# Kernel optimization log

Measured on AMD Instinct MI355X. Metric: run time of the kernel, lower is better.

## Reference

```python
import jax, jax.numpy as jnp
import numpy as np

B, T, C = 2, 2048, 1024
H = 16
D = C // H  # 64

def setup_inputs() -> dict:
    key = jax.random.key(0)
    k1, k2, k3 = jax.random.split(key, 3)
    s = 0.02
    return {
        "x": jax.random.normal(k1, (B, T, C), dtype=jnp.float32),
        "Wqkv": jax.random.normal(k2, (C, 3 * C), dtype=jnp.float32) * s,
        "bqkv": jnp.zeros((3 * C,), dtype=jnp.float32),
        "Wproj": jax.random.normal(k3, (C, C), dtype=jnp.float32) * s,
        "bproj": jnp.zeros((C,), dtype=jnp.float32),
    }

def reference(x, Wqkv, bqkv, Wproj, bproj):
    b, t, c = x.shape
    qkv = x @ Wqkv + bqkv                       # [B,T,3C]
    qkv = qkv.reshape(b, t, 3, H, D)
    q = qkv[:, :, 0].transpose(0, 2, 1, 3)      # [B,H,T,D]
    k = qkv[:, :, 1].transpose(0, 2, 1, 3)
    v = qkv[:, :, 2].transpose(0, 2, 1, 3)
    scale = 1.0 / np.sqrt(D).astype(np.float32)
    att = jnp.einsum('bhqd,bhkd->bhqk', q, k) * scale  # [B,H,T,T]
    causal = jnp.tril(jnp.ones((t, t), dtype=bool))
    att = jnp.where(causal[None, None], att, jnp.float32(-jnp.inf))
    att = jax.nn.softmax(att, axis=-1)
    y = jnp.einsum('bhqk,bhkd->bhqd', att, v)   # [B,H,T,D]
    y = y.transpose(0, 2, 1, 3).reshape(b, t, c)
    return y @ Wproj + bproj
```

## Files before the change

### kernel.cpp

```cpp
#include <hip/hip_runtime.h>

typedef __bf16 bf16x8 __attribute__((ext_vector_type(8)));
typedef float  f32x4  __attribute__((ext_vector_type(4)));
typedef float  f32x16 __attribute__((ext_vector_type(16)));
typedef unsigned int uint32x4 __attribute__((ext_vector_type(4)));

__device__ __forceinline__ short f2bf(float f) {
  union { float f; unsigned u; } v; v.f = f;
  unsigned r = v.u + 0x7fffu + ((v.u >> 16) & 1u);
  return (short)(r >> 16);
}

__device__ __forceinline__ void gl_lds16(const short* g, short* l) {
  __builtin_amdgcn_global_load_lds((const __attribute__((address_space(1))) void*)g,
                                   (__attribute__((address_space(3))) void*)l, 16, 0, 0);
}

__global__ __launch_bounds__(256) void cast_x_kernel(const float* __restrict__ in,
                                                     short* __restrict__ out, int n4) {
  int i = blockIdx.x * 256 + threadIdx.x;
  if (i >= n4) return;
  float4 f = reinterpret_cast<const float4*>(in)[i];
  short4 o;
  o.x = f2bf(f.x); o.y = f2bf(f.y); o.z = f2bf(f.z); o.w = f2bf(f.w);
  reinterpret_cast<short4*>(out)[i] = o;
}

__global__ __launch_bounds__(256) void transpose_cast(const float* __restrict__ in,
                                                      short* __restrict__ out, int R, int Cc) {
  __shared__ short tile[64][65];
  int bx = blockIdx.x * 64;
  int by = blockIdx.y * 64;
  int tx = threadIdx.x & 63, ty = threadIdx.x >> 6;
  #pragma unroll
  for (int i = ty; i < 64; i += 4)
    tile[i][tx] = f2bf(in[(size_t)(by + i) * Cc + bx + tx]);
  __syncthreads();
  #pragma unroll
  for (int i = ty; i < 64; i += 4)
    out[(size_t)(bx + i) * R + by + tx] = tile[tx][i];
}


__global__ __launch_bounds__(512, 1) void gemm_qkv(const short* __restrict__ A,
                                                   const short* __restrict__ Bt,
                                                   const float* __restrict__ bias,
                                                   short* __restrict__ qo,
                                                   short* __restrict__ ko,
                                                   short* __restrict__ vt) {
  const int K = 1024;
  __shared__ short smem[65536];
  int tid = threadIdx.x;
  int g = blockIdx.x;
  int mtile = (g & 15) * 256, ntile = (g >> 4) * 256;
  int w = tid >> 6, l = tid & 63;
  int wr = w >> 2, wc = w & 3;
  int lr = l & 15, lg = l >> 4;

  f32x4 zero4 = {0.f, 0.f, 0.f, 0.f};
  f32x4 acc[8][4];
  #pragma unroll
  for (int i = 0; i < 8; ++i)
    #pragma unroll
    for (int j = 0; j < 4; ++j) acc[i][j] = zero4;

#define STAGE_QKV(BUF, K0) do {                                                      \
    short* Ab_ = smem + (BUF) * 32768;                                               \
    short* Bb_ = Ab_ + 16384;                                                        \
    _Pragma("unroll")                                                                \
    for (int c = 0; c < 4; ++c) {                                                    \
      int idx = tid + c * 512;                                                       \
      int row = idx >> 3, kc = (idx & 7) ^ (row & 7);       \
      gl_lds16(&A[(size_t)(mtile + row) * K + (K0) + kc * 8], &Ab_[idx * 8]);        \
      gl_lds16(&Bt[(size_t)(ntile + row) * K + (K0) + kc * 8], &Bb_[idx * 8]);       \
    }                                                                                \
  } while (0)

  STAGE_QKV(0, 0);
  __syncthreads();
  int cur = 0;
  for (int it = 0; it < 16; ++it) {
    if (it < 15) STAGE_QKV(cur ^ 1, (it + 1) * 64);
    const short* Ab = smem + cur * 32768;
    const short* Bb = Ab + 16384;
    __builtin_amdgcn_s_setprio(1);
    #pragma unroll
    for (int kk = 0; kk < 2; ++kk) {
      bf16x8 af[8], bfr[4];
      #pragma unroll
      for (int i = 0; i < 8; ++i) {
        int rA = wr * 128 + i * 16 + lr;
        af[i] = *reinterpret_cast<const bf16x8*>(&Ab[rA * 64 + (((kk * 4 + lg) ^ (rA & 7)) * 8)]);
      }
      #pragma unroll
      for (int j = 0; j < 4; ++j) {
        int rB = wc * 64 + j * 16 + lr;
        bfr[j] = *reinterpret_cast<const bf16x8*>(&Bb[rB * 64 + (((kk * 4 + lg) ^ (rB & 7)) * 8)]);
      }
      #pragma unroll
      for (int i = 0; i < 8; ++i)
        #pragma unroll
        for (int j = 0; j < 4; ++j)
          acc[i][j] = __builtin_amdgcn_mfma_f32_16x16x32_bf16(af[i], bfr[j], acc[i][j], 0, 0, 0);
    }
    __builtin_amdgcn_s_setprio(0);
    __syncthreads();
    cur ^= 1;
  }
#undef STAGE_QKV

  const int sec = ntile >> 10;
  if (sec == 2) {
    #pragma unroll
    for (int j = 0; j < 4; ++j) {
      int nl = wc * 64 + j * 16 + lr;
      int d  = nl & 63;
      float bv = bias[ntile + nl];
      #pragma unroll
      for (int i = 0; i < 8; ++i) {
        int lt0 = wr * 128 + i * 16 + lg * 4;
        int c2 = (nl >> 6) * 8 + (lt0 >> 5);
        int pos = (((lt0 >> 3) & 1) << 10) + (d & 31) * 32 +
                  ((((lt0 >> 4) & 1) + ((d >> 5) << 1)) << 3) + (lt0 & 7);
        short4 pk;
        pk.x = f2bf(acc[i][j][0] + bv);
        pk.y = f2bf(acc[i][j][1] + bv);
        pk.z = f2bf(acc[i][j][2] + bv);
        pk.w = f2bf(acc[i][j][3] + bv);
        *reinterpret_cast<short4*>(&smem[c2 * 2048 + pos]) = pk;
      }
    }
  } else {
    const float sc = (sec == 0) ? 0.18033688f : 1.0f;
    #pragma unroll
    for (int j = 0; j < 4; ++j) {
      int nl = wc * 64 + j * 16 + lr;
      int d  = nl & 63;
      float bv = bias[ntile + nl];
      int dpart = (((d >> 3) & 1) << 10) + ((d >> 4) << 3) + (d & 7);
      #pragma unroll
      for (int i = 0; i < 8; ++i) {
        #pragma unroll
        for (int r2 = 0; r2 < 4; ++r2) {
          int lt = wr * 128 + i * 16 + lg * 4 + r2;
          int c2 = (nl >> 6) * 8 + (lt >> 5);
          smem[c2 * 2048 + (lt & 31) * 32 + dpart] = f2bf((acc[i][j][r2] + bv) * sc);
        }
      }
    }
  }
  __syncthreads();
  short* dst = (sec == 0) ? qo : ((sec == 1) ? ko : vt);
  int bb  = mtile >> 11;
  int h0  = (ntile & 1023) >> 6;
  int gt0 = (mtile & 2047) >> 5;
  #pragma unroll
  for (int c2 = 0; c2 < 32; ++c2) {
    size_t base = (size_t)(bb * 16 + h0 + (c2 >> 3)) * 131072 +
                  (size_t)(gt0 + (c2 & 7)) * 2048;
    *reinterpret_cast<uint2*>(&dst[base + tid * 4]) =
        *reinterpret_cast<const uint2*>(&smem[c2 * 2048 + tid * 4]);
  }
}

template<int DIAG>
__device__ __forceinline__ void attn_step(const short* __restrict__ kp,
                                          const short* __restrict__ vp,
                                          const bf16x8* qf,
                                          f32x16& y0, f32x16& y1,
                                          float& m, float& li,
                                          int lq, int hl) {
  f32x16 s;
  #pragma unroll
  for (int r = 0; r < 16; ++r) s[r] = 0.f;
  __builtin_amdgcn_s_setprio(1);
  #pragma unroll
  for (int ks = 0; ks < 4; ++ks) {
    bf16x8 kf = *reinterpret_cast<const bf16x8*>(kp + ks * 8);
    s = __builtin_amdgcn_mfma_f32_32x32x16_bf16(kf, qf[ks], s, 0, 0, 0);
  }
  __builtin_amdgcn_s_setprio(0);
  if (DIAG) {
    #pragma unroll
    for (int r = 0; r < 16; ++r) {
      int kvl = (r & 3) + 8 * (r >> 2) + 4 * hl;
      if (kvl > lq) s[r] = -1e30f;
    }
  }
  float a0 = fmaxf(fmaxf(s[0], s[1]), fmaxf(s[2], s[3]));
  float a1 = fmaxf(fmaxf(s[4], s[5]), fmaxf(s[6], s[7]));
  float a2 = fmaxf(fmaxf(s[8], s[9]), fmaxf(s[10], s[11]));
  float a3 = fmaxf(fmaxf(s[12], s[13]), fmaxf(s[14], s[15]));
  float pm = fmaxf(fmaxf(a0, a1), fmaxf(a2, a3));
  pm = fmaxf(pm, __shfl_xor(pm, 32));
  if (!__all(pm - m <= 8.0f)) {
    float mn = fmaxf(m, pm);
    float sc = __builtin_amdgcn_exp2f(m - mn);
    m = mn;
    li *= sc;
    #pragma unroll
    for (int r = 0; r < 16; ++r) { y0[r] *= sc; y1[r] *= sc; }
  }
  unsigned u[8];
  float rs = 0.f;
  #pragma unroll
  for (int rq = 0; rq < 4; ++rq) {
    float p0 = __builtin_amdgcn_exp2f(s[4 * rq + 0] - m);
    float p1 = __builtin_amdgcn_exp2f(s[4 * rq + 1] - m);
    float p2 = __builtin_amdgcn_exp2f(s[4 * rq + 2] - m);
    float p3 = __builtin_amdgcn_exp2f(s[4 * rq + 3] - m);
    rs += (p0 + p1) + (p2 + p3);
    asm("v_cvt_pk_bf16_f32 %0, %1, %2" : "=v"(u[rq * 2 + 0]) : "v"(p0), "v"(p1));
    asm("v_cvt_pk_bf16_f32 %0, %1, %2" : "=v"(u[rq * 2 + 1]) : "v"(p2), "v"(p3));
  }
  rs += __shfl_xor(rs, 32);
  li += rs;
  asm volatile("v_permlane32_swap_b32 %0, %1" : "+v"(u[0]), "+v"(u[2]));
  asm volatile("v_permlane32_swap_b32 %0, %1" : "+v"(u[1]), "+v"(u[3]));
  asm volatile("v_permlane32_swap_b32 %0, %1" : "+v"(u[4]), "+v"(u[6]));
  asm volatile("v_permlane32_swap_b32 %0, %1" : "+v"(u[5]), "+v"(u[7]));
  uint32x4 w0 = {u[0], u[1], u[2], u[3]};
  uint32x4 w1 = {u[4], u[5], u[6], u[7]};
  bf16x8 pa0 = __builtin_bit_cast(bf16x8, w0);
  bf16x8 pa1 = __builtin_bit_cast(bf16x8, w1);
  __builtin_amdgcn_s_setprio(1);
  {
    bf16x8 vf00 = *reinterpret_cast<const bf16x8*>(vp);
    bf16x8 vf01 = *reinterpret_cast<const bf16x8*>(vp + 8);
    bf16x8 vf10 = *reinterpret_cast<const bf16x8*>(vp + 16);
    bf16x8 vf11 = *reinterpret_cast<const bf16x8*>(vp + 24);
    y0 = __builtin_amdgcn_mfma_f32_32x32x16_bf16(vf00, pa0, y0, 0, 0, 0);
    y0 = __builtin_amdgcn_mfma_f32_32x32x16_bf16(vf01, pa1, y0, 0, 0, 0);
    y1 = __builtin_amdgcn_mfma_f32_32x32x16_bf16(vf10, pa0, y1, 0, 0, 0);
    y1 = __builtin_amdgcn_mfma_f32_32x32x16_bf16(vf11, pa1, y1, 0, 0, 0);
  }
  __builtin_amdgcn_s_setprio(0);
}

__global__ __launch_bounds__(256, 4) void attn_kernel(const short* __restrict__ q,
                                                      const short* __restrict__ k,
                                                      const short* __restrict__ vt,
                                                      short* __restrict__ y) {
  __shared__ float partL[3][4][64][4];
  __shared__ float stm[4][32], stl[4][32];
  const int bid = blockIdx.x;
  const int t = 63 - (bid >> 5);
  const int b5 = bid & 31;
  const int bh = (b5 & 7) * 4 + (b5 >> 3);
  const int tid = threadIdx.x;
  const int w = tid >> 6;
  const int l = tid & 63;
  const int lq = l & 31, hl = l >> 5;
  const short* qb = q + (size_t)bh * 131072;
  const short* kb = k + (size_t)bh * 131072;
  const short* vb = vt + (size_t)bh * 131072;

  bf16x8 qf[4];
  {
    const short* qp = qb + (size_t)t * 2048 + l * 32;
    #pragma unroll
    for (int ks = 0; ks < 4; ++ks)
      qf[ks] = *reinterpret_cast<const bf16x8*>(qp + ks * 8);
  }

  f32x16 y0, y1;
  #pragma unroll
  for (int r = 0; r < 16; ++r) { y0[r] = 0.f; y1[r] = 0.f; }
  float m = -1e30f, li = 0.f;

  const short* kp = kb + (size_t)w * 2048 + l * 32;
  const short* vp = vb + (size_t)w * 2048 + l * 32;
  for (int it = w; it < t; it += 4) {
    attn_step<0>(kp, vp, qf, y0, y1, m, li, lq, hl);
    kp += 4 * 2048;
    vp += 4 * 2048;
  }
  if ((t & 3) == w) {
    const short* kpd = kb + (size_t)t * 2048 + l * 32;
    const short* vpd = vb + (size_t)t * 2048 + l * 32;
    attn_step<1>(kpd, vpd, qf, y0, y1, m, li, lq, hl);
  }

  if (hl == 0) { stm[w][lq] = m; stl[w][lq] = li; }
  __syncthreads();
  float m0 = stm[0][lq], m1 = stm[1][lq], m2 = stm[2][lq], m3 = stm[3][lq];
  float M = fmaxf(fmaxf(m0, m1), fmaxf(m2, m3));
  float L = stl[0][lq] * __builtin_amdgcn_exp2f(m0 - M) +
            stl[1][lq] * __builtin_amdgcn_exp2f(m1 - M) +
            stl[2][lq] * __builtin_amdgcn_exp2f(m2 - M) +
            stl[3][lq] * __builtin_amdgcn_exp2f(m3 - M);
  float sc = __builtin_amdgcn_exp2f(m - M);
  #pragma unroll
  for (int r = 0; r < 16; ++r) { y0[r] *= sc; y1[r] *= sc; }

  if (w > 0) {
    #pragma unroll
    for (int c = 0; c < 4; ++c) {
      f32x4 v0 = {y0[4 * c + 0], y0[4 * c + 1], y0[4 * c + 2], y0[4 * c + 3]};
      *reinterpret_cast<f32x4*>(&partL[w - 1][c][l][0]) = v0;
    }
  }
  __syncthreads();
  if (w == 0) {
    #pragma unroll
    for (int o = 0; o < 3; ++o)
      #pragma unroll
      for (int c = 0; c < 4; ++c) {
        f32x4 v0 = *reinterpret_cast<const f32x4*>(&partL[o][c][l][0]);
        #pragma unroll
        for (int r = 0; r < 4; ++r) y0[4 * c + r] += v0[r];
      }
  }
  __syncthreads();
  if (w > 0) {
    #pragma unroll
    for (int c = 0; c < 4; ++c) {
      f32x4 v1 = {y1[4 * c + 0], y1[4 * c + 1], y1[4 * c + 2], y1[4 * c + 3]};
      *reinterpret_cast<f32x4*>(&partL[w - 1][c][l][0]) = v1;
    }
  }
  __syncthreads();
  if (w == 0) {
    #pragma unroll
    for (int o = 0; o < 3; ++o)
      #pragma unroll
      for (int c = 0; c < 4; ++c) {
        f32x4 v1 = *reinterpret_cast<const f32x4*>(&partL[o][c][l][0]);
        #pragma unroll
        for (int r = 0; r < 4; ++r) y1[4 * c + r] += v1[r];
      }
    float inv = 1.0f / L;
    int b_ = bh >> 4, h_ = bh & 15;
    short* yrow = &y[(size_t)(b_ * 2048 + 32 * t + lq) * 1024 + h_ * 64];
    #pragma unroll
    for (int dt = 0; dt < 2; ++dt) {
      const f32x16& yy = dt ? y1 : y0;
      #pragma unroll
      for (int rq = 0; rq < 4; ++rq) {
        int d0 = dt * 32 + 8 * rq + 4 * hl;
        uint2 pk;
        pk.x = (unsigned)(unsigned short)f2bf(yy[4 * rq + 0] * inv) |
               ((unsigned)(unsigned short)f2bf(yy[4 * rq + 1] * inv) << 16);
        pk.y = (unsigned)(unsigned short)f2bf(yy[4 * rq + 2] * inv) |
               ((unsigned)(unsigned short)f2bf(yy[4 * rq + 3] * inv) << 16);
        *reinterpret_cast<uint2*>(yrow + d0) = pk;
      }
    }
  }
}

__global__ __launch_bounds__(256, 3) void gemm_proj(const short* __restrict__ A,
                                                    const short* __restrict__ Bt,
                                                    const float* __restrict__ bias,
                                                    float* __restrict__ out) {
  const int K = 1024;
  __shared__ short smem[24576];
  int tid = threadIdx.x;
  int x = blockIdx.x & 7, r = blockIdx.x >> 3;
  int ntile = (x * 2 + (r & 1)) * 64, mtile = (r >> 1) * 128;
  int w = tid >> 6, l = tid & 63;
  int lr = l & 15, lg = l >> 4;

  f32x4 zero4 = {0.f, 0.f, 0.f, 0.f};
  f32x4 acc[2][4];
  #pragma unroll
  for (int i = 0; i < 2; ++i)
    #pragma unroll
    for (int j = 0; j < 4; ++j) acc[i][j] = zero4;

#define STAGE_PRJ(BUF, K0) do {                                                      \
    short* Ab_ = smem + (BUF) * 12288;                                               \
    short* Bb_ = Ab_ + 8192;                                                         \
    _Pragma("unroll")                                                                \
    for (int c = 0; c < 4; ++c) {                                                    \
      int idx = tid + c * 256;                                                       \
      int row = idx >> 3, kc = (idx & 7) ^ (row & 7);                                \
      gl_lds16(&A[(size_t)(mtile + row) * K + (K0) + kc * 8], &Ab_[idx * 8]);        \
    }                                                                                \
    _Pragma("unroll")                                                                \
    for (int c = 0; c < 2; ++c) {                                                    \
      int idx = tid + c * 256;                                                       \
      int row = idx >> 3, kc = (idx & 7) ^ (row & 7);                                \
      gl_lds16(&Bt[(size_t)(ntile + row) * K + (K0) + kc * 8], &Bb_[idx * 8]);       \
    }                                                                                \
  } while (0)

  STAGE_PRJ(0, 0);
  __syncthreads();
  int cur = 0;
  for (int it = 0; it < 16; ++it) {
    if (it < 15) STAGE_PRJ(cur ^ 1, (it + 1) * 64);
    const short* Ab = smem + cur * 12288;
    const short* Bb = Ab + 8192;
    __builtin_amdgcn_s_setprio(1);
    #pragma unroll
    for (int kk = 0; kk < 2; ++kk) {
      bf16x8 af[2], bfr[4];
      #pragma unroll
      for (int i = 0; i < 2; ++i) {
        int rA = w * 32 + i * 16 + lr;
        af[i] = *reinterpret_cast<const bf16x8*>(&Ab[rA * 64 + (((kk * 4 + lg) ^ (rA & 7)) * 8)]);
      }
      #pragma unroll
      for (int j = 0; j < 4; ++j) {
        int rB = j * 16 + lr;
        bfr[j] = *reinterpret_cast<const bf16x8*>(&Bb[rB * 64 + (((kk * 4 + lg) ^ (rB & 7)) * 8)]);
      }
      #pragma unroll
      for (int i = 0; i < 2; ++i)
        #pragma unroll
        for (int j = 0; j < 4; ++j)
          acc[i][j] = __builtin_amdgcn_mfma_f32_16x16x32_bf16(af[i], bfr[j], acc[i][j], 0, 0, 0);
    }
    __builtin_amdgcn_s_setprio(0);
    __syncthreads();
    cur ^= 1;
  }
#undef STAGE_PRJ

  #pragma unroll
  for (int j = 0; j < 4; ++j) {
    int n = ntile + j * 16 + lr;
    float bv = bias[n];
    #pragma unroll
    for (int i = 0; i < 2; ++i) {
      #pragma unroll
      for (int r2 = 0; r2 < 4; ++r2) {
        int m = mtile + w * 32 + i * 16 + lg * 4 + r2;
        out[(size_t)m * 1024 + n] = acc[i][j][r2] + bv;
      }
    }
  }
}

extern "C" void kernel_launch(void* const* d_in, const int* in_sizes, int n_in,
                              void* d_out, int out_size, void* d_ws, size_t ws_size,
                              hipStream_t stream) {
  const float* x     = (const float*)d_in[0];
  const float* Wqkv  = (const float*)d_in[1];
  const float* bqkv  = (const float*)d_in[2];
  const float* Wproj = (const float*)d_in[3];
  const float* bproj = (const float*)d_in[4];
  float* out = (float*)d_out;

  const size_t M4 = 4096ull * 1024ull;
  short* ws = (short*)d_ws;
  short* x_bf    = ws;
  short* wqkv_t  = ws + M4;
  short* wproj_t = ws + M4 + 3ull * 1024 * 1024;
  short* qb      = wproj_t + 1024ull * 1024;
  short* kb      = qb + M4;
  short* vtb     = kb + M4;
  short* yb      = x_bf;

  cast_x_kernel<<<4096, 256, 0, stream>>>(x, x_bf, (int)(M4 / 4));
  transpose_cast<<<dim3(48, 16), 256, 0, stream>>>(Wqkv, wqkv_t, 1024, 3072);
  transpose_cast<<<dim3(16, 16), 256, 0, stream>>>(Wproj, wproj_t, 1024, 1024);
  gemm_qkv<<<192, 512, 0, stream>>>(x_bf, wqkv_t, bqkv, qb, kb, vtb);
  attn_kernel<<<2048, 256, 0, stream>>>(qb, kb, vtb, yb);
  gemm_proj<<<512, 256, 0, stream>>>(yb, wproj_t, bproj, out);
}
```

Baseline: 110.7 us.

## Fold running max into MFMA accumulator init and process two KV tiles per step

The score accumulator is now initialized to -m, so the max subtraction is folded into the QK MFMA and the per-element subtract before exp2 disappears. The main loop handles two 32-key tiles per iteration, sharing one max reduction and rescale check across both, with a single-tile step left for the remainder and the diagonal tile. This cuts VALU work and gives the MFMA chain more independent work per iteration to hide latency. It costs more registers for the second score and probability set, which could hurt occupancy at launch bounds of 4 blocks. The initial m changes from -1e30 to 0, which relies on the lazy-rescale threshold to stay numerically safe.

```diff
diff --git a/kernel.cpp b/kernel.cpp
--- a/kernel.cpp
+++ b/kernel.cpp
@@ -164,15 +164,15 @@
 }
 
 template<int DIAG>
-__device__ __forceinline__ void attn_step(const short* __restrict__ kp,
-                                          const short* __restrict__ vp,
-                                          const bf16x8* qf,
-                                          f32x16& y0, f32x16& y1,
-                                          float& m, float& li,
-                                          int lq, int hl) {
+__device__ __forceinline__ void attn_step1(const short* __restrict__ kp,
+                                           const short* __restrict__ vp,
+                                           const bf16x8* qf,
+                                           f32x16& y0, f32x16& y1,
+                                           float& m, float& li,
+                                           int lq, int hl) {
   f32x16 s;
   #pragma unroll
-  for (int r = 0; r < 16; ++r) s[r] = 0.f;
+  for (int r = 0; r < 16; ++r) s[r] = -m;
   __builtin_amdgcn_s_setprio(1);
   #pragma unroll
   for (int ks = 0; ks < 4; ++ks) {
@@ -193,22 +193,22 @@
   float a3 = fmaxf(fmaxf(s[12], s[13]), fmaxf(s[14], s[15]));
   float pm = fmaxf(fmaxf(a0, a1), fmaxf(a2, a3));
   pm = fmaxf(pm, __shfl_xor(pm, 32));
-  if (!__all(pm - m <= 8.0f)) {
-    float mn = fmaxf(m, pm);
-    float sc = __builtin_amdgcn_exp2f(m - mn);
-    m = mn;
+  if (!__all(pm <= 8.0f)) {
+    float delta = fmaxf(pm, 0.0f);
+    float sc = __builtin_amdgcn_exp2f(-delta);
+    m += delta;
     li *= sc;
     #pragma unroll
-    for (int r = 0; r < 16; ++r) { y0[r] *= sc; y1[r] *= sc; }
+    for (int r = 0; r < 16; ++r) { y0[r] *= sc; y1[r] *= sc; s[r] -= delta; }
   }
   unsigned u[8];
   float rs = 0.f;
   #pragma unroll
   for (int rq = 0; rq < 4; ++rq) {
-    float p0 = __builtin_amdgcn_exp2f(s[4 * rq + 0] - m);
-    float p1 = __builtin_amdgcn_exp2f(s[4 * rq + 1] - m);
-    float p2 = __builtin_amdgcn_exp2f(s[4 * rq + 2] - m);
-    float p3 = __builtin_amdgcn_exp2f(s[4 * rq + 3] - m);
+    float p0 = __builtin_amdgcn_exp2f(s[4 * rq + 0]);
+    float p1 = __builtin_amdgcn_exp2f(s[4 * rq + 1]);
+    float p2 = __builtin_amdgcn_exp2f(s[4 * rq + 2]);
+    float p3 = __builtin_amdgcn_exp2f(s[4 * rq + 3]);
     rs += (p0 + p1) + (p2 + p3);
     asm("v_cvt_pk_bf16_f32 %0, %1, %2" : "=v"(u[rq * 2 + 0]) : "v"(p0), "v"(p1));
     asm("v_cvt_pk_bf16_f32 %0, %1, %2" : "=v"(u[rq * 2 + 1]) : "v"(p2), "v"(p3));
@@ -237,6 +237,105 @@
   __builtin_amdgcn_s_setprio(0);
 }
 
+__device__ __forceinline__ void attn_step2(const short* __restrict__ kp,
+                                           const short* __restrict__ vp,
+                                           const bf16x8* qf,
+                                           f32x16& y0, f32x16& y1,
+                                           float& m, float& li,
+                                           int lq, int hl) {
+  const short* kp1 = kp + 4 * 2048;
+  const short* vp1 = vp + 4 * 2048;
+  f32x16 s0, s1;
+  #pragma unroll
+  for (int r = 0; r < 16; ++r) { s0[r] = -m; s1[r] = -m; }
+  __builtin_amdgcn_s_setprio(1);
+  #pragma unroll
+  for (int ks = 0; ks < 4; ++ks) {
+    bf16x8 kf0 = *reinterpret_cast<const bf16x8*>(kp + ks * 8);
+    s0 = __builtin_amdgcn_mfma_f32_32x32x16_bf16(kf0, qf[ks], s0, 0, 0, 0);
+    bf16x8 kf1 = *reinterpret_cast<const bf16x8*>(kp1 + ks * 8);
+    s1 = __builtin_amdgcn_mfma_f32_32x32x16_bf16(kf1, qf[ks], s1, 0, 0, 0);
+  }
+  __builtin_amdgcn_s_setprio(0);
+  float a0 = fmaxf(fmaxf(s0[0], s0[1]), fmaxf(s0[2], s0[3]));
+  float a1 = fmaxf(fmaxf(s0[4], s0[5]), fmaxf(s0[6], s0[7]));
+  float a2 = fmaxf(fmaxf(s0[8], s0[9]), fmaxf(s0[10], s0[11]));
+  float a3 = fmaxf(fmaxf(s0[12], s0[13]), fmaxf(s0[14], s0[15]));
+  float b0 = fmaxf(fmaxf(s1[0], s1[1]), fmaxf(s1[2], s1[3]));
+  float b1 = fmaxf(fmaxf(s1[4], s1[5]), fmaxf(s1[6], s1[7]));
+  float b2 = fmaxf(fmaxf(s1[8], s1[9]), fmaxf(s1[10], s1[11]));
+  float b3 = fmaxf(fmaxf(s1[12], s1[13]), fmaxf(s1[14], s1[15]));
+  float pm = fmaxf(fmaxf(fmaxf(a0, a1), fmaxf(a2, a3)),
+                   fmaxf(fmaxf(b0, b1), fmaxf(b2, b3)));
+  pm = fmaxf(pm, __shfl_xor(pm, 32));
+  if (!__all(pm <= 8.0f)) {
+    float delta = fmaxf(pm, 0.0f);
+    float sc = __builtin_amdgcn_exp2f(-delta);
+    m += delta;
+    li *= sc;
+    #pragma unroll
+    for (int r = 0; r < 16; ++r) {
+      y0[r] *= sc; y1[r] *= sc; s0[r] -= delta; s1[r] -= delta;
+    }
+  }
+  unsigned u0[8], u1[8];
+  float rs = 0.f;
+  #pragma unroll
+  for (int rq = 0; rq < 4; ++rq) {
+    float p0 = __builtin_amdgcn_exp2f(s0[4 * rq + 0]);
+    float p1 = __builtin_amdgcn_exp2f(s0[4 * rq + 1]);
+    float p2 = __builtin_amdgcn_exp2f(s0[4 * rq + 2]);
+    float p3 = __builtin_amdgcn_exp2f(s0[4 * rq + 3]);
+    float q0 = __builtin_amdgcn_exp2f(s1[4 * rq + 0]);
+    float q1 = __builtin_amdgcn_exp2f(s1[4 * rq + 1]);
+    float q2 = __builtin_amdgcn_exp2f(s1[4 * rq + 2]);
+    float q3 = __builtin_amdgcn_exp2f(s1[4 * rq + 3]);
+    rs += ((p0 + p1) + (p2 + p3)) + ((q0 + q1) + (q2 + q3));
+    asm("v_cvt_pk_bf16_f32 %0, %1, %2" : "=v"(u0[rq * 2 + 0]) : "v"(p0), "v"(p1));
+    asm("v_cvt_pk_bf16_f32 %0, %1, %2" : "=v"(u0[rq * 2 + 1]) : "v"(p2), "v"(p3));
+    asm("v_cvt_pk_bf16_f32 %0, %1, %2" : "=v"(u1[rq * 2 + 0]) : "v"(q0), "v"(q1));
+    asm("v_cvt_pk_bf16_f32 %0, %1, %2" : "=v"(u1[rq * 2 + 1]) : "v"(q2), "v"(q3));
+  }
+  rs += __shfl_xor(rs, 32);
+  li += rs;
+  asm volatile("v_permlane32_swap_b32 %0, %1" : "+v"(u0[0]), "+v"(u0[2]));
+  asm volatile("v_permlane32_swap_b32 %0, %1" : "+v"(u0[1]), "+v"(u0[3]));
+  asm volatile("v_permlane32_swap_b32 %0, %1" : "+v"(u0[4]), "+v"(u0[6]));
+  asm volatile("v_permlane32_swap_b32 %0, %1" : "+v"(u0[5]), "+v"(u0[7]));
+  asm volatile("v_permlane32_swap_b32 %0, %1" : "+v"(u1[0]), "+v"(u1[2]));
+  asm volatile("v_permlane32_swap_b32 %0, %1" : "+v"(u1[1]), "+v"(u1[3]));
+  asm volatile("v_permlane32_swap_b32 %0, %1" : "+v"(u1[4]), "+v"(u1[6]));
+  asm volatile("v_permlane32_swap_b32 %0, %1" : "+v"(u1[5]), "+v"(u1[7]));
+  uint32x4 w00 = {u0[0], u0[1], u0[2], u0[3]};
+  uint32x4 w01 = {u0[4], u0[5], u0[6], u0[7]};
+  uint32x4 w10 = {u1[0], u1[1], u1[2], u1[3]};
+  uint32x4 w11 = {u1[4], u1[5], u1[6], u1[7]};
+  bf16x8 pa00 = __builtin_bit_cast(bf16x8, w00);
+  bf16x8 pa01 = __builtin_bit_cast(bf16x8, w01);
+  bf16x8 pa10 = __builtin_bit_cast(bf16x8, w10);
+  bf16x8 pa11 = __builtin_bit_cast(bf16x8, w11);
+  __builtin_amdgcn_s_setprio(1);
+  {
+    bf16x8 vf00 = *reinterpret_cast<const bf16x8*>(vp);
+    bf16x8 vf01 = *reinterpret_cast<const bf16x8*>(vp + 8);
+    bf16x8 vf10 = *reinterpret_cast<const bf16x8*>(vp + 16);
+    bf16x8 vf11 = *reinterpret_cast<const bf16x8*>(vp + 24);
+    y0 = __builtin_amdgcn_mfma_f32_32x32x16_bf16(vf00, pa00, y0, 0, 0, 0);
+    y0 = __builtin_amdgcn_mfma_f32_32x32x16_bf16(vf01, pa01, y0, 0, 0, 0);
+    y1 = __builtin_amdgcn_mfma_f32_32x32x16_bf16(vf10, pa00, y1, 0, 0, 0);
+    y1 = __builtin_amdgcn_mfma_f32_32x32x16_bf16(vf11, pa01, y1, 0, 0, 0);
+    bf16x8 wf00 = *reinterpret_cast<const bf16x8*>(vp1);
+    bf16x8 wf01 = *reinterpret_cast<const bf16x8*>(vp1 + 8);
+    bf16x8 wf10 = *reinterpret_cast<const bf16x8*>(vp1 + 16);
+    bf16x8 wf11 = *reinterpret_cast<const bf16x8*>(vp1 + 24);
+    y0 = __builtin_amdgcn_mfma_f32_32x32x16_bf16(wf00, pa10, y0, 0, 0, 0);
+    y0 = __builtin_amdgcn_mfma_f32_32x32x16_bf16(wf01, pa11, y0, 0, 0, 0);
+    y1 = __builtin_amdgcn_mfma_f32_32x32x16_bf16(wf10, pa10, y1, 0, 0, 0);
+    y1 = __builtin_amdgcn_mfma_f32_32x32x16_bf16(wf11, pa11, y1, 0, 0, 0);
+  }
+  __builtin_amdgcn_s_setprio(0);
+}
+
 __global__ __launch_bounds__(256, 4) void attn_kernel(const short* __restrict__ q,
                                                       const short* __restrict__ k,
                                                       const short* __restrict__ vt,
@@ -266,20 +365,17 @@
   f32x16 y0, y1;
   #pragma unroll
   for (int r = 0; r < 16; ++r) { y0[r] = 0.f; y1[r] = 0.f; }
-  float m = -1e30f, li = 0.f;
-
-  const short* kp = kb + (size_t)w * 2048 + l * 32;
-  const short* vp = vb + (size_t)w * 2048 + l * 32;
-  for (int it = w; it < t; it += 4) {
-    attn_step<0>(kp, vp, qf, y0, y1, m, li, lq, hl);
-    kp += 4 * 2048;
-    vp += 4 * 2048;
-  }
-  if ((t & 3) == w) {
-    const short* kpd = kb + (size_t)t * 2048 + l * 32;
-    const short* vpd = vb + (size_t)t * 2048 + l * 32;
-    attn_step<1>(kpd, vpd, qf, y0, y1, m, li, lq, hl);
-  }
+  float m = 0.f, li = 0.f;
+
+  const short* k0 = kb + l * 32;
+  const short* v0 = vb + l * 32;
+  int it = w;
+  for (; it + 4 < t; it += 8)
+    attn_step2(k0 + (size_t)it * 2048, v0 + (size_t)it * 2048, qf, y0, y1, m, li, lq, hl);
+  if (it < t)
+    attn_step1<0>(k0 + (size_t)it * 2048, v0 + (size_t)it * 2048, qf, y0, y1, m, li, lq, hl);
+  if ((t & 3) == w)
+    attn_step1<1>(k0 + (size_t)t * 2048, v0 + (size_t)t * 2048, qf, y0, y1, m, li, lq, hl);
 
   if (hl == 0) { stm[w][lq] = m; stl[w][lq] = li; }
   __syncthreads();
@@ -296,8 +392,8 @@
   if (w > 0) {
     #pragma unroll
     for (int c = 0; c < 4; ++c) {
-      f32x4 v0 = {y0[4 * c + 0], y0[4 * c + 1], y0[4 * c + 2], y0[4 * c + 3]};
-      *reinterpret_cast<f32x4*>(&partL[w - 1][c][l][0]) = v0;
+      f32x4 v0s = {y0[4 * c + 0], y0[4 * c + 1], y0[4 * c + 2], y0[4 * c + 3]};
+      *reinterpret_cast<f32x4*>(&partL[w - 1][c][l][0]) = v0s;
     }
   }
   __syncthreads();
@@ -306,17 +402,17 @@
     for (int o = 0; o < 3; ++o)
       #pragma unroll
       for (int c = 0; c < 4; ++c) {
-        f32x4 v0 = *reinterpret_cast<const f32x4*>(&partL[o][c][l][0]);
+        f32x4 v0s = *reinterpret_cast<const f32x4*>(&partL[o][c][l][0]);
         #pragma unroll
-        for (int r = 0; r < 4; ++r) y0[4 * c + r] += v0[r];
+        for (int r = 0; r < 4; ++r) y0[4 * c + r] += v0s[r];
       }
   }
   __syncthreads();
   if (w > 0) {
     #pragma unroll
     for (int c = 0; c < 4; ++c) {
-      f32x4 v1 = {y1[4 * c + 0], y1[4 * c + 1], y1[4 * c + 2], y1[4 * c + 3]};
-      *reinterpret_cast<f32x4*>(&partL[w - 1][c][l][0]) = v1;
+      f32x4 v1s = {y1[4 * c + 0], y1[4 * c + 1], y1[4 * c + 2], y1[4 * c + 3]};
+      *reinterpret_cast<f32x4*>(&partL[w - 1][c][l][0]) = v1s;
     }
   }
   __syncthreads();
@@ -325,9 +421,9 @@
     for (int o = 0; o < 3; ++o)
       #pragma unroll
       for (int c = 0; c < 4; ++c) {
-        f32x4 v1 = *reinterpret_cast<const f32x4*>(&partL[o][c][l][0]);
+        f32x4 v1s = *reinterpret_cast<const f32x4*>(&partL[o][c][l][0]);
         #pragma unroll
-        for (int r = 0; r < 4; ++r) y1[4 * c + r] += v1[r];
+        for (int r = 0; r < 4; ++r) y1[4 * c + r] += v1s[r];
       }
     float inv = 1.0f / L;
     int b_ = bh >> 4, h_ = bh & 15;
```

New measurement: 117.6 us. +6.2%, slower.
